# Kernel tuning notes

Measured on AMD Instinct MI355X. Metric: run time of the kernel, lower is better.

Reference implementation:

```python
import jax, jax.numpy as jnp
import numpy as np

T, B, OBS, A, P, NB, H = 32, 256, 1024, 16, 600, 601, 128


def setup_inputs() -> dict:
    key = jax.random.key(0)
    ks = jax.random.split(key, 32)
    f32 = jnp.float32

    def rn(k, shape, scale):
        return jax.random.normal(k, shape, dtype=f32) * scale

    hh = 1.0 / np.sqrt(H)
    inp = {
        "obs_seq": rn(ks[0], (T, B, OBS), 1.0),
        # backbone MLP (512, 512)
        "bb_w1": rn(ks[1], (OBS, 512), 1.0 / np.sqrt(OBS)), "bb_b1": jnp.zeros((512,), f32),
        "bb_w2": rn(ks[2], (512, 512), 1.0 / np.sqrt(512)), "bb_b2": jnp.zeros((512,), f32),
        # feedforward heads (final layers init std=0.01, bias 0 per module)
        "pol_w": rn(ks[3], (512, A), 0.01), "pol_b": jnp.zeros((A,), f32),
        "y_w": rn(ks[4], (512, P), 0.01), "y_b": jnp.zeros((P,), f32),
        "ci_w": rn(ks[5], (512, H), 1.0 / np.sqrt(512)), "ci_b": jnp.zeros((H,), f32),
        # LSTMCell(A, 128): gate order i,f,g,o as in torch
        "w_ih": rn(ks[6], (A, 4 * H), hh), "w_hh": rn(ks[7], (H, 4 * H), hh),
        "b_ih": rn(ks[8], (4 * H,), hh), "b_hh": rn(ks[9], (4 * H,), hh),
        # z / q / aux_pi MLPs: Linear(128,128) -> ReLU -> Linear(128, out)
        "z_w1": rn(ks[10], (H, H), hh), "z_b1": jnp.zeros((H,), f32),
        "z_w2": rn(ks[11], (H, P), 0.01), "z_b2": jnp.zeros((P,), f32),
        "q_w1": rn(ks[12], (H, H), hh), "q_b1": jnp.zeros((H,), f32),
        "q_w2": rn(ks[13], (H, NB), 0.01), "q_b2": jnp.zeros((NB,), f32),
        "a_w1": rn(ks[14], (H, H), hh), "a_b1": jnp.zeros((H,), f32),
        "a_w2": rn(ks[15], (H, A), 0.01), "a_b2": jnp.zeros((A,), f32),
    }
    return inp


def reference(obs_seq, bb_w1, bb_b1, bb_w2, bb_b2, pol_w, pol_b, y_w, y_b,
              ci_w, ci_b, w_ih, w_hh, b_ih, b_hh,
              z_w1, z_b1, z_w2, z_b2, q_w1, q_b1, q_w2, q_b2,
              a_w1, a_b1, a_w2, a_b2):
    Tn, Bn = obs_seq.shape[:2]
    x = obs_seq.reshape(Tn * Bn, -1)  # feedforward across time: fold T into batch
    emb = jax.nn.relu(jax.nn.relu(x @ bb_w1 + bb_b1) @ bb_w2 + bb_b2)  # [N,512]
    logits = emb @ pol_w + pol_b  # [N,A]
    y = emb @ y_w + y_b           # [N,P]
    c0 = emb @ ci_w + ci_b        # [N,H]
    h0 = jnp.tanh(c0)

    # one_hot(a) @ W_ih^T == row a of W_ih (input-to-gate contribution per action)
    in_gates = w_ih + b_ih  # [A, 4H]

    def step(carry, ig):
        h, c = carry
        g = ig + h @ w_hh + b_hh  # [N,4H]
        i, f, gg, o = jnp.split(g, 4, axis=-1)  # torch gate order i,f,g,o
        c = jax.nn.sigmoid(f) * c + jax.nn.sigmoid(i) * jnp.tanh(gg)
        h = jax.nn.sigmoid(o) * jnp.tanh(c)
        return (h, c), h

    _, h_all = jax.lax.scan(step, (h0, c0), in_gates)  # [A, N, H]

    def mlp(hx, w1, b1, w2, b2):
        return jax.nn.relu(hx @ w1 + b1) @ w2 + b2

    def to_tba(arr):
        Aa, N, D = arr.shape
        return arr.reshape(Aa, Tn, Bn, D).transpose(1, 2, 0, 3)  # [T,B,A,D]

    z = to_tba(mlp(h_all, z_w1, z_b1, z_w2, z_b2))
    q = to_tba(mlp(h_all, q_w1, q_b1, q_w2, q_b2))
    aux_pi = to_tba(mlp(h_all, a_w1, a_b1, a_w2, a_b2))
    return (logits.reshape(Tn, Bn, -1), y.reshape(Tn, Bn, -1), z, q, aux_pi)
```

## Files before the change

### kernel.cpp

```cpp
#include <hip/hip_runtime.h>
#include <stdint.h>

typedef short bf16x8 __attribute__((ext_vector_type(8)));
typedef float f32x4 __attribute__((ext_vector_type(4)));
typedef unsigned short u16x4 __attribute__((ext_vector_type(4)));

__device__ __forceinline__ unsigned short f2b(float f) {
  union { float f; unsigned u; } v; v.f = f;
  unsigned r = v.u + 0x7fffu + ((v.u >> 16) & 1u);
  return (unsigned short)(r >> 16);
}
__device__ __forceinline__ float fsigm(float x) { return 1.f / (1.f + __expf(-x)); }
__device__ __forceinline__ float ftanh(float x) {
  float t = __expf(-2.f * fabsf(x));
  float r = (1.f - t) / (1.f + t);
  return copysignf(r, x);
}

struct TD { const float* in; unsigned short* out; int R, C; };
struct TDs { TD d[12]; };

__global__ __launch_bounds__(256) void tconv_all(TDs ds) {
  TD t = ds.d[blockIdx.z];
  int c0 = blockIdx.x * 32, r0 = blockIdx.y * 32;
  if (c0 >= t.C || r0 >= t.R) return;
  __shared__ float tl[32][33];
  int tx = threadIdx.x & 31, ty = threadIdx.x >> 5;
  #pragma unroll
  for (int i = 0; i < 32; i += 8) {
    int r = r0 + ty + i, c = c0 + tx;
    tl[ty + i][tx] = (r < t.R && c < t.C) ? t.in[(size_t)r * t.C + c] : 0.f;
  }
  __syncthreads();
  #pragma unroll
  for (int i = 0; i < 32; i += 8) {
    int c = c0 + ty + i, r = r0 + tx;
    if (c < t.C && r < t.R) t.out[(size_t)c * t.R + r] = f2b(tl[tx][ty + i]);
  }
}

__global__ __launch_bounds__(256) void conv_k(const float* __restrict__ in,
                                              unsigned short* __restrict__ out, int n) {
  int i = (blockIdx.x * 256 + threadIdx.x) * 8;
  if (i >= n) return;
  float4 a = *(const float4*)(in + i);
  float4 b = *(const float4*)(in + i + 4);
  bf16x8 v;
  v[0] = (short)f2b(a.x); v[1] = (short)f2b(a.y); v[2] = (short)f2b(a.z); v[3] = (short)f2b(a.w);
  v[4] = (short)f2b(b.x); v[5] = (short)f2b(b.y); v[6] = (short)f2b(b.z); v[7] = (short)f2b(b.w);
  *(bf16x8*)(out + i) = v;
}

template <int ACT, bool OBF16>
__global__ __launch_bounds__(256) void gemm_k(const unsigned short* __restrict__ A,
                                              const unsigned short* __restrict__ BT,
                                              const float* __restrict__ bias,
                                              void* __restrict__ Cp,
                                              int M, int N, int K, int ldC) {
  __shared__ unsigned short As[64][40];
  __shared__ unsigned short Bs[64][40];
  const int tid = threadIdx.x;
  const int n0 = blockIdx.x * 64;
  const int m0 = blockIdx.y * 64;
  const int wid = tid >> 6, lane = tid & 63;
  const int wm = (wid >> 1) * 32, wn = (wid & 1) * 32;
  const int lr = lane & 15, lk = lane >> 4;
  const int sr = tid >> 2, sc = (tid & 3) * 8;

  f32x4 acc[2][2] = {};

  for (int k0 = 0; k0 < K; k0 += 32) {
    *(bf16x8*)&As[sr][sc] = *(const bf16x8*)(A + (size_t)(m0 + sr) * K + k0 + sc);
    {
      int n = n0 + sr;
      bf16x8 v = {};
      if (n < N) v = *(const bf16x8*)(BT + (size_t)n * K + k0 + sc);
      *(bf16x8*)&Bs[sr][sc] = v;
    }
    __syncthreads();
    bf16x8 af[2], bfr[2];
    #pragma unroll
    for (int mi = 0; mi < 2; mi++) af[mi] = *(const bf16x8*)&As[wm + mi * 16 + lr][lk * 8];
    #pragma unroll
    for (int ni = 0; ni < 2; ni++) bfr[ni] = *(const bf16x8*)&Bs[wn + ni * 16 + lr][lk * 8];
    #pragma unroll
    for (int mi = 0; mi < 2; mi++)
      #pragma unroll
      for (int ni = 0; ni < 2; ni++)
        acc[mi][ni] = __builtin_amdgcn_mfma_f32_16x16x32_bf16(af[mi], bfr[ni], acc[mi][ni], 0, 0, 0);
    __syncthreads();
  }

  #pragma unroll
  for (int mi = 0; mi < 2; mi++)
    #pragma unroll
    for (int ni = 0; ni < 2; ni++) {
      int col = n0 + wn + ni * 16 + lr;
      if (col >= N) continue;
      float bv = bias[col];
      #pragma unroll
      for (int r = 0; r < 4; r++) {
        int row = m0 + wm + mi * 16 + lk * 4 + r;
        float v = acc[mi][ni][r] + bv;
        if (ACT == 1) v = fmaxf(v, 0.f);
        if (OBF16) ((unsigned short*)Cp)[(size_t)row * ldC + col] = f2b(v);
        else       ((float*)Cp)[(size_t)row * ldC + col] = v;
      }
    }
}

__global__ __launch_bounds__(1024) void lstm_k(const float* __restrict__ c0,
                                               const unsigned short* __restrict__ whhT,
                                               const float* __restrict__ w_ih,
                                               const float* __restrict__ b_ih,
                                               const float* __restrict__ b_hh,
                                               unsigned short* __restrict__ h_all) {
  __shared__ float G[32][516];
  __shared__ float cst[32][128];
  __shared__ unsigned short hst[32][136];
  const int tid = threadIdx.x, lane = tid & 63, wid = tid >> 6;
  const int r0 = blockIdx.x * 32;
  const int lr = lane & 15, lk = lane >> 4;

  {
    int r = tid >> 5, j4 = (tid & 31) * 4;
    float4 c4 = *(const float4*)(c0 + (size_t)(r0 + r) * 128 + j4);
    *(f32x4*)&cst[r][j4] = f32x4{c4.x, c4.y, c4.z, c4.w};
    u16x4 h4;
    h4[0] = f2b(ftanh(c4.x)); h4[1] = f2b(ftanh(c4.y));
    h4[2] = f2b(ftanh(c4.z)); h4[3] = f2b(ftanh(c4.w));
    *(u16x4*)&hst[r][j4] = h4;
  }
  __syncthreads();

  for (int a = 0; a < 16; a++) {
    f32x4 acc[2][2] = {};
    #pragma unroll
    for (int ks = 0; ks < 4; ks++) {
      bf16x8 af0 = *(const bf16x8*)&hst[lr][ks * 32 + lk * 8];
      bf16x8 af1 = *(const bf16x8*)&hst[16 + lr][ks * 32 + lk * 8];
      #pragma unroll
      for (int nj = 0; nj < 2; nj++) {
        int col = wid * 32 + nj * 16 + lr;
        bf16x8 bv = *(const bf16x8*)(whhT + (size_t)col * 128 + ks * 32 + lk * 8);
        acc[0][nj] = __builtin_amdgcn_mfma_f32_16x16x32_bf16(af0, bv, acc[0][nj], 0, 0, 0);
        acc[1][nj] = __builtin_amdgcn_mfma_f32_16x16x32_bf16(af1, bv, acc[1][nj], 0, 0, 0);
      }
    }
    #pragma unroll
    for (int mi = 0; mi < 2; mi++)
      #pragma unroll
      for (int nj = 0; nj < 2; nj++)
        #pragma unroll
        for (int rr = 0; rr < 4; rr++)
          G[mi * 16 + lk * 4 + rr][wid * 32 + nj * 16 + lr] = acc[mi][nj][rr];
    __syncthreads();

    const float* ig = w_ih + a * 512;
    #pragma unroll
    for (int it = 0; it < 4; it++) {
      int e = tid + it * 1024;
      int r = e >> 7, j = e & 127;
      float gi = G[r][j]       + ig[j]       + b_ih[j]       + b_hh[j];
      float gf = G[r][j + 128] + ig[j + 128] + b_ih[j + 128] + b_hh[j + 128];
      float gg = G[r][j + 256] + ig[j + 256] + b_ih[j + 256] + b_hh[j + 256];
      float go = G[r][j + 384] + ig[j + 384] + b_ih[j + 384] + b_hh[j + 384];
      float c = cst[r][j];
      float cn = fsigm(gf) * c + fsigm(gi) * ftanh(gg);
      float h = fsigm(go) * ftanh(cn);
      cst[r][j] = cn;
      unsigned short hb = f2b(h);
      hst[r][j] = hb;
      h_all[((size_t)(r0 + r) * 16 + a) * 128 + j] = hb;
    }
    __syncthreads();
  }
}

__global__ __launch_bounds__(256, 4) void heads_k(
    const unsigned short* __restrict__ hall,
    const unsigned short* __restrict__ w1cat,
    const unsigned short* __restrict__ w2cat,
    const float* __restrict__ zb1, const float* __restrict__ qb1, const float* __restrict__ ab1,
    const float* __restrict__ zb2, const float* __restrict__ qb2, const float* __restrict__ ab2,
    float* __restrict__ oz, float* __restrict__ oq, float* __restrict__ oa) {
  __shared__ unsigned short hs[64][136];
  __shared__ unsigned short hd[64][136];
  const int tid = threadIdx.x;
  const int r0 = blockIdx.x * 64;
  const int lane = tid & 63, wid = tid >> 6;
  const int lr = lane & 15, lk = lane >> 4;

  {
    int row = tid >> 2, cb = (tid & 3) * 8;
    #pragma unroll
    for (int it = 0; it < 4; it++) {
      int col = cb + it * 32;
      *(bf16x8*)&hs[row][col] = *(const bf16x8*)(hall + (size_t)(r0 + row) * 128 + col);
    }
  }
  __syncthreads();

  const float* B1a[3] = {zb1, qb1, ab1};
  const float* B2a[3] = {zb2, qb2, ab2};
  float*       OOa[3] = {oz, oq, oa};

  #pragma unroll
  for (int hi = 0; hi < 3; hi++) {
    const int NF = (hi == 0) ? 38 : (hi == 1) ? 38 : 1;
    const int Nh = (hi == 0) ? 600 : (hi == 1) ? 601 : 16;
    const int so = (hi == 0) ? 0 : (hi == 1) ? 600 : 1201;
    const float* b1 = B1a[hi];
    const float* b2 = B2a[hi];
    float* Oh = OOa[hi];

    {
      bf16x8 w1v[2][4];
      #pragma unroll
      for (int j = 0; j < 2; j++) {
        int col = (wid * 2 + j) * 16 + lr;
        #pragma unroll
        for (int ks = 0; ks < 4; ks++)
          w1v[j][ks] = *(const bf16x8*)(w1cat + (size_t)(hi * 128 + col) * 128 + ks * 32 + lk * 8);
      }
      f32x4 hacc[2][4] = {};
      #pragma unroll
      for (int ks = 0; ks < 4; ks++) {
        bf16x8 av[4];
        #pragma unroll
        for (int mi = 0; mi < 4; mi++)
          av[mi] = *(const bf16x8*)&hs[mi * 16 + lr][ks * 32 + lk * 8];
        #pragma unroll
        for (int j = 0; j < 2; j++)
          #pragma unroll
          for (int mi = 0; mi < 4; mi++)
            hacc[j][mi] = __builtin_amdgcn_mfma_f32_16x16x32_bf16(av[mi], w1v[j][ks], hacc[j][mi], 0, 0, 0);
      }
      #pragma unroll
      for (int j = 0; j < 2; j++) {
        int col = (wid * 2 + j) * 16 + lr;
        float bb = b1[col];
        #pragma unroll
        for (int mi = 0; mi < 4; mi++)
          #pragma unroll
          for (int rr = 0; rr < 4; rr++)
            hd[mi * 16 + lk * 4 + rr][col] = f2b(fmaxf(hacc[j][mi][rr] + bb, 0.f));
      }
    }
    __syncthreads();

    {
      bf16x8 hda[4][4];
      #pragma unroll
      for (int mi = 0; mi < 4; mi++)
        #pragma unroll
        for (int ks = 0; ks < 4; ks++)
          hda[mi][ks] = *(const bf16x8*)&hd[mi * 16 + lr][ks * 32 + lk * 8];

      bf16x8 bvA[4], bvB[4];
      int f = wid;
      if (f < NF) {
        int bc = min(f * 16 + lr, Nh - 1);
        #pragma unroll
        for (int ks = 0; ks < 4; ks++)
          bvA[ks] = *(const bf16x8*)(w2cat + (size_t)(so + bc) * 128 + ks * 32 + lk * 8);
      }
      for (; f < NF; f += 4) {
        int fn = f + 4;
        if (fn < NF) {
          int bc = min(fn * 16 + lr, Nh - 1);
          #pragma unroll
          for (int ks = 0; ks < 4; ks++)
            bvB[ks] = *(const bf16x8*)(w2cat + (size_t)(so + bc) * 128 + ks * 32 + lk * 8);
        }
        f32x4 oacc[4] = {};
        #pragma unroll
        for (int ks = 0; ks < 4; ks++)
          #pragma unroll
          for (int mi = 0; mi < 4; mi++)
            oacc[mi] = __builtin_amdgcn_mfma_f32_16x16x32_bf16(hda[mi][ks], bvA[ks], oacc[mi], 0, 0, 0);
        int col = f * 16 + lr;
        if (col < Nh) {
          float bb = b2[col];
          #pragma unroll
          for (int mi = 0; mi < 4; mi++)
            #pragma unroll
            for (int rr = 0; rr < 4; rr++)
              Oh[(size_t)(r0 + mi * 16 + lk * 4 + rr) * Nh + col] = oacc[mi][rr] + bb;
        }
        #pragma unroll
        for (int ks = 0; ks < 4; ks++) bvA[ks] = bvB[ks];
      }
    }
    __syncthreads();
  }
}

extern "C" void kernel_launch(void* const* d_in, const int* in_sizes, int n_in,
                              void* d_out, int out_size, void* d_ws, size_t ws_size,
                              hipStream_t stream) {
  const float* obs   = (const float*)d_in[0];
  const float* bb_w1 = (const float*)d_in[1];
  const float* bb_b1 = (const float*)d_in[2];
  const float* bb_w2 = (const float*)d_in[3];
  const float* bb_b2 = (const float*)d_in[4];
  const float* pol_w = (const float*)d_in[5];
  const float* pol_b = (const float*)d_in[6];
  const float* y_w   = (const float*)d_in[7];
  const float* y_b   = (const float*)d_in[8];
  const float* ci_w  = (const float*)d_in[9];
  const float* ci_b  = (const float*)d_in[10];
  const float* w_ih  = (const float*)d_in[11];
  const float* w_hh  = (const float*)d_in[12];
  const float* b_ih  = (const float*)d_in[13];
  const float* b_hh  = (const float*)d_in[14];
  const float* z_w1  = (const float*)d_in[15];
  const float* z_b1  = (const float*)d_in[16];
  const float* z_w2  = (const float*)d_in[17];
  const float* z_b2  = (const float*)d_in[18];
  const float* q_w1  = (const float*)d_in[19];
  const float* q_b1  = (const float*)d_in[20];
  const float* q_w2  = (const float*)d_in[21];
  const float* q_b2  = (const float*)d_in[22];
  const float* a_w1  = (const float*)d_in[23];
  const float* a_b1  = (const float*)d_in[24];
  const float* a_w2  = (const float*)d_in[25];
  const float* a_b2  = (const float*)d_in[26];

  float* out = (float*)d_out;
  float* out_logits = out;
  float* out_y      = out + 131072;
  float* out_z      = out + 5046272;
  float* out_q      = out + 83689472;
  float* out_a      = out + 162463744;

  uint8_t* ws = (uint8_t*)d_ws;
  size_t off = 0;
  auto alc = [&](size_t bytes) -> void* {
    void* p = ws + off;
    off = (off + bytes + 255) & ~(size_t)255;
    return p;
  };
  unsigned short* W1T  = (unsigned short*)alc((size_t)512 * 1024 * 2);
  unsigned short* W2T  = (unsigned short*)alc((size_t)512 * 512 * 2);
  unsigned short* polT = (unsigned short*)alc((size_t)16 * 512 * 2);
  unsigned short* yT   = (unsigned short*)alc((size_t)600 * 512 * 2);
  unsigned short* ciT  = (unsigned short*)alc((size_t)128 * 512 * 2);
  unsigned short* whhT = (unsigned short*)alc((size_t)512 * 128 * 2);
  unsigned short* zw1T = (unsigned short*)alc((size_t)128 * 128 * 2);
  unsigned short* qw1T = (unsigned short*)alc((size_t)128 * 128 * 2);
  unsigned short* aw1T = (unsigned short*)alc((size_t)128 * 128 * 2);
  unsigned short* zw2T = (unsigned short*)alc((size_t)600 * 128 * 2);
  unsigned short* qw2T = (unsigned short*)alc((size_t)601 * 128 * 2);
  unsigned short* aw2T = (unsigned short*)alc((size_t)16 * 128 * 2);
  unsigned short* obsb = (unsigned short*)alc((size_t)8192 * 1024 * 2);
  unsigned short* hid1 = (unsigned short*)alc((size_t)8192 * 512 * 2);
  unsigned short* emb  = (unsigned short*)alc((size_t)8192 * 512 * 2);
  float*          c0b  = (float*)alc((size_t)8192 * 128 * 4);
  unsigned short* hall = (unsigned short*)alc((size_t)8192 * 16 * 128 * 2);
  (void)ws_size; (void)in_sizes; (void)n_in; (void)out_size;

  dim3 B256(256);

  TDs td;
  td.d[0]  = {bb_w1, W1T, 1024, 512};
  td.d[1]  = {bb_w2, W2T, 512, 512};
  td.d[2]  = {pol_w, polT, 512, 16};
  td.d[3]  = {y_w,   yT,   512, 600};
  td.d[4]  = {ci_w,  ciT,  512, 128};
  td.d[5]  = {w_hh,  whhT, 128, 512};
  td.d[6]  = {z_w1,  zw1T, 128, 128};
  td.d[7]  = {z_w2,  zw2T, 128, 600};
  td.d[8]  = {q_w1,  qw1T, 128, 128};
  td.d[9]  = {q_w2,  qw2T, 128, 601};
  td.d[10] = {a_w1,  aw1T, 128, 128};
  td.d[11] = {a_w2,  aw2T, 128, 16};
  tconv_all<<<dim3(19, 32, 12), B256, 0, stream>>>(td);

  conv_k<<<dim3(4096), B256, 0, stream>>>(obs, obsb, 8192 * 1024);

  gemm_k<1, true><<<dim3(8, 128), B256, 0, stream>>>(obsb, W1T, bb_b1, hid1, 8192, 512, 1024, 512);
  gemm_k<1, true><<<dim3(8, 128), B256, 0, stream>>>(hid1, W2T, bb_b2, emb,  8192, 512, 512,  512);
  gemm_k<0, false><<<dim3(1, 128),  B256, 0, stream>>>(emb, polT, pol_b, out_logits, 8192, 16,  512, 16);
  gemm_k<0, false><<<dim3(10, 128), B256, 0, stream>>>(emb, yT,   y_b,   out_y,      8192, 600, 512, 600);
  gemm_k<0, false><<<dim3(2, 128),  B256, 0, stream>>>(emb, ciT,  ci_b,  c0b,        8192, 128, 512, 128);
  lstm_k<<<dim3(256), dim3(1024), 0, stream>>>(c0b, whhT, w_ih, b_ih, b_hh, hall);
  heads_k<<<dim3(2048), B256, 0, stream>>>(hall,
                                           zw1T, zw2T,
                                           z_b1, q_b1, a_b1,
                                           z_b2, q_b2, a_b2,
                                           out_z, out_q, out_a);
}
```

Before: 481.7 us.

## Restructure heads kernel to single-wave blocks with transposed MFMA and vector stores

The LSTM kernel now keeps its W_hh fragments in registers across all 16 steps and precomputes the bias sums and per-step input-gate values per thread. The heads kernel is rebuilt around 64-thread blocks, each handling 32 rows. Each block reads h directly from global memory, swaps the MFMA operand order so every lane produces 4 contiguous output columns, and writes those with 16-byte vector stores instead of scattered scalar stores. It also drops the block-level barriers in favour of a wave-local LDS wait. The cost is more blocks, with each block reloading W1 and W2, and more VGPR pressure from the register-resident weights.

```diff
diff --git a/kernel.cpp b/kernel.cpp
--- a/kernel.cpp
+++ b/kernel.cpp
@@ -122,6 +122,20 @@
   const int r0 = blockIdx.x * 32;
   const int lr = lane & 15, lk = lane >> 4;
 
+  bf16x8 wv[2][4];
+  #pragma unroll
+  for (int nj = 0; nj < 2; nj++)
+    #pragma unroll
+    for (int ks = 0; ks < 4; ks++)
+      wv[nj][ks] = *(const bf16x8*)(whhT + (size_t)(wid * 32 + nj * 16 + lr) * 128 + ks * 32 + lk * 8);
+
+  const int j = tid & 127;
+  const int rb = tid >> 7;
+  const float bs0 = b_ih[j]       + b_hh[j];
+  const float bs1 = b_ih[j + 128] + b_hh[j + 128];
+  const float bs2 = b_ih[j + 256] + b_hh[j + 256];
+  const float bs3 = b_ih[j + 384] + b_hh[j + 384];
+
   {
     int r = tid >> 5, j4 = (tid & 31) * 4;
     float4 c4 = *(const float4*)(c0 + (size_t)(r0 + r) * 128 + j4);
@@ -141,10 +155,8 @@
       bf16x8 af1 = *(const bf16x8*)&hst[16 + lr][ks * 32 + lk * 8];
       #pragma unroll
       for (int nj = 0; nj < 2; nj++) {
-        int col = wid * 32 + nj * 16 + lr;
-        bf16x8 bv = *(const bf16x8*)(whhT + (size_t)col * 128 + ks * 32 + lk * 8);
-        acc[0][nj] = __builtin_amdgcn_mfma_f32_16x16x32_bf16(af0, bv, acc[0][nj], 0, 0, 0);
-        acc[1][nj] = __builtin_amdgcn_mfma_f32_16x16x32_bf16(af1, bv, acc[1][nj], 0, 0, 0);
+        acc[0][nj] = __builtin_amdgcn_mfma_f32_16x16x32_bf16(af0, wv[nj][ks], acc[0][nj], 0, 0, 0);
+        acc[1][nj] = __builtin_amdgcn_mfma_f32_16x16x32_bf16(af1, wv[nj][ks], acc[1][nj], 0, 0, 0);
       }
     }
     #pragma unroll
@@ -157,14 +169,14 @@
     __syncthreads();
 
     const float* ig = w_ih + a * 512;
+    const float ig0 = ig[j], ig1 = ig[j + 128], ig2 = ig[j + 256], ig3 = ig[j + 384];
     #pragma unroll
     for (int it = 0; it < 4; it++) {
-      int e = tid + it * 1024;
-      int r = e >> 7, j = e & 127;
-      float gi = G[r][j]       + ig[j]       + b_ih[j]       + b_hh[j];
-      float gf = G[r][j + 128] + ig[j + 128] + b_ih[j + 128] + b_hh[j + 128];
-      float gg = G[r][j + 256] + ig[j + 256] + b_ih[j + 256] + b_hh[j + 256];
-      float go = G[r][j + 384] + ig[j + 384] + b_ih[j + 384] + b_hh[j + 384];
+      int r = rb + it * 8;
+      float gi = G[r][j]       + ig0 + bs0;
+      float gf = G[r][j + 128] + ig1 + bs1;
+      float gg = G[r][j + 256] + ig2 + bs2;
+      float go = G[r][j + 384] + ig3 + bs3;
       float c = cst[r][j];
       float cn = fsigm(gf) * c + fsigm(gi) * ftanh(gg);
       float h = fsigm(go) * ftanh(cn);
@@ -177,29 +189,17 @@
   }
 }
 
-__global__ __launch_bounds__(256, 4) void heads_k(
+__global__ __launch_bounds__(64, 4) void heads_k(
     const unsigned short* __restrict__ hall,
     const unsigned short* __restrict__ w1cat,
     const unsigned short* __restrict__ w2cat,
     const float* __restrict__ zb1, const float* __restrict__ qb1, const float* __restrict__ ab1,
     const float* __restrict__ zb2, const float* __restrict__ qb2, const float* __restrict__ ab2,
     float* __restrict__ oz, float* __restrict__ oq, float* __restrict__ oa) {
-  __shared__ unsigned short hs[64][136];
-  __shared__ unsigned short hd[64][136];
-  const int tid = threadIdx.x;
-  const int r0 = blockIdx.x * 64;
-  const int lane = tid & 63, wid = tid >> 6;
+  __shared__ unsigned short hp[32][136];
+  const int lane = threadIdx.x & 63;
   const int lr = lane & 15, lk = lane >> 4;
-
-  {
-    int row = tid >> 2, cb = (tid & 3) * 8;
-    #pragma unroll
-    for (int it = 0; it < 4; it++) {
-      int col = cb + it * 32;
-      *(bf16x8*)&hs[row][col] = *(const bf16x8*)(hall + (size_t)(r0 + row) * 128 + col);
-    }
-  }
-  __syncthreads();
+  const int r0 = blockIdx.x * 32;
 
   const float* B1a[3] = {zb1, qb1, ab1};
   const float* B2a[3] = {zb2, qb2, ab2};
@@ -207,92 +207,102 @@
 
   #pragma unroll
   for (int hi = 0; hi < 3; hi++) {
-    const int NF = (hi == 0) ? 38 : (hi == 1) ? 38 : 1;
-    const int Nh = (hi == 0) ? 600 : (hi == 1) ? 601 : 16;
-    const int so = (hi == 0) ? 0 : (hi == 1) ? 600 : 1201;
+    const int Nh    = (hi == 0) ? 600 : (hi == 1) ? 601 : 16;
+    const int so    = (hi == 0) ? 0 : (hi == 1) ? 600 : 1201;
+    const int NFULL = Nh >> 4;
+    const int TAIL  = Nh & 15;
     const float* b1 = B1a[hi];
     const float* b2 = B2a[hi];
     float* Oh = OOa[hi];
 
     {
-      bf16x8 w1v[2][4];
-      #pragma unroll
-      for (int j = 0; j < 2; j++) {
-        int col = (wid * 2 + j) * 16 + lr;
+      bf16x8 av[2][4];
+      #pragma unroll
+      for (int jf = 0; jf < 2; jf++)
         #pragma unroll
         for (int ks = 0; ks < 4; ks++)
-          w1v[j][ks] = *(const bf16x8*)(w1cat + (size_t)(hi * 128 + col) * 128 + ks * 32 + lk * 8);
-      }
-      f32x4 hacc[2][4] = {};
-      #pragma unroll
-      for (int ks = 0; ks < 4; ks++) {
-        bf16x8 av[4];
-        #pragma unroll
-        for (int mi = 0; mi < 4; mi++)
-          av[mi] = *(const bf16x8*)&hs[mi * 16 + lr][ks * 32 + lk * 8];
-        #pragma unroll
-        for (int j = 0; j < 2; j++)
+          av[jf][ks] = *(const bf16x8*)(hall + (size_t)(r0 + jf * 16 + lr) * 128 + ks * 32 + lk * 8);
+      #pragma unroll
+      for (int nf = 0; nf < 8; nf++) {
+        bf16x8 w1v[4];
+        #pragma unroll
+        for (int ks = 0; ks < 4; ks++)
+          w1v[ks] = *(const bf16x8*)(w1cat + (size_t)(hi * 128 + nf * 16 + lr) * 128 + ks * 32 + lk * 8);
+        f32x4 hacc[2] = {};
+        #pragma unroll
+        for (int ks = 0; ks < 4; ks++)
           #pragma unroll
-          for (int mi = 0; mi < 4; mi++)
-            hacc[j][mi] = __builtin_amdgcn_mfma_f32_16x16x32_bf16(av[mi], w1v[j][ks], hacc[j][mi], 0, 0, 0);
-      }
-      #pragma unroll
-      for (int j = 0; j < 2; j++) {
-        int col = (wid * 2 + j) * 16 + lr;
-        float bb = b1[col];
-        #pragma unroll
-        for (int mi = 0; mi < 4; mi++)
+          for (int jf = 0; jf < 2; jf++)
+            hacc[jf] = __builtin_amdgcn_mfma_f32_16x16x32_bf16(w1v[ks], av[jf][ks], hacc[jf], 0, 0, 0);
+        f32x4 bb = *(const f32x4*)(b1 + nf * 16 + lk * 4);
+        #pragma unroll
+        for (int jf = 0; jf < 2; jf++) {
+          u16x4 h4;
           #pragma unroll
           for (int rr = 0; rr < 4; rr++)
-            hd[mi * 16 + lk * 4 + rr][col] = f2b(fmaxf(hacc[j][mi][rr] + bb, 0.f));
+            h4[rr] = f2b(fmaxf(hacc[jf][rr] + bb[rr], 0.f));
+          *(u16x4*)&hp[jf * 16 + lr][nf * 16 + lk * 4] = h4;
+        }
       }
     }
-    __syncthreads();
-
+    asm volatile("s_waitcnt lgkmcnt(0)" ::: "memory");
+    __builtin_amdgcn_sched_barrier(0);
+
+    bf16x8 hv[2][4];
+    #pragma unroll
+    for (int jf = 0; jf < 2; jf++)
+      #pragma unroll
+      for (int ks = 0; ks < 4; ks++)
+        hv[jf][ks] = *(const bf16x8*)&hp[jf * 16 + lr][ks * 32 + lk * 8];
+
+    bf16x8 wA[4], wB[4];
     {
-      bf16x8 hda[4][4];
-      #pragma unroll
-      for (int mi = 0; mi < 4; mi++)
+      int rowb = min(lr, Nh - 1);
+      #pragma unroll
+      for (int ks = 0; ks < 4; ks++)
+        wA[ks] = *(const bf16x8*)(w2cat + (size_t)(so + rowb) * 128 + ks * 32 + lk * 8);
+    }
+    const int NFT = NFULL + (TAIL ? 1 : 0);
+    for (int fo = 0; fo < NFULL; fo++) {
+      int fn = fo + 1;
+      if (fn < NFT) {
+        int rowb = min(fn * 16 + lr, Nh - 1);
         #pragma unroll
         for (int ks = 0; ks < 4; ks++)
-          hda[mi][ks] = *(const bf16x8*)&hd[mi * 16 + lr][ks * 32 + lk * 8];
-
-      bf16x8 bvA[4], bvB[4];
-      int f = wid;
-      if (f < NF) {
-        int bc = min(f * 16 + lr, Nh - 1);
-        #pragma unroll
-        for (int ks = 0; ks < 4; ks++)
-          bvA[ks] = *(const bf16x8*)(w2cat + (size_t)(so + bc) * 128 + ks * 32 + lk * 8);
+          wB[ks] = *(const bf16x8*)(w2cat + (size_t)(so + rowb) * 128 + ks * 32 + lk * 8);
       }
-      for (; f < NF; f += 4) {
-        int fn = f + 4;
-        if (fn < NF) {
-          int bc = min(fn * 16 + lr, Nh - 1);
-          #pragma unroll
-          for (int ks = 0; ks < 4; ks++)
-            bvB[ks] = *(const bf16x8*)(w2cat + (size_t)(so + bc) * 128 + ks * 32 + lk * 8);
+      f32x4 oacc[2] = {};
+      #pragma unroll
+      for (int ks = 0; ks < 4; ks++)
+        #pragma unroll
+        for (int jf = 0; jf < 2; jf++)
+          oacc[jf] = __builtin_amdgcn_mfma_f32_16x16x32_bf16(wA[ks], hv[jf][ks], oacc[jf], 0, 0, 0);
+      f32x4 bb = *(const f32x4*)(b2 + fo * 16 + lk * 4);
+      #pragma unroll
+      for (int jf = 0; jf < 2; jf++) {
+        f32x4 v = oacc[jf] + bb;
+        float* p = Oh + (size_t)(r0 + jf * 16 + lr) * Nh + fo * 16 + lk * 4;
+        __builtin_memcpy(p, &v, 16);
+      }
+      #pragma unroll
+      for (int ks = 0; ks < 4; ks++) wA[ks] = wB[ks];
+    }
+    if (TAIL) {
+      f32x4 oacc[2] = {};
+      #pragma unroll
+      for (int ks = 0; ks < 4; ks++)
+        #pragma unroll
+        for (int jf = 0; jf < 2; jf++)
+          oacc[jf] = __builtin_amdgcn_mfma_f32_16x16x32_bf16(wA[ks], hv[jf][ks], oacc[jf], 0, 0, 0);
+      #pragma unroll
+      for (int jf = 0; jf < 2; jf++)
+        #pragma unroll
+        for (int rr = 0; rr < 4; rr++) {
+          int col = NFULL * 16 + lk * 4 + rr;
+          if (col < Nh)
+            Oh[(size_t)(r0 + jf * 16 + lr) * Nh + col] = oacc[jf][rr] + b2[col];
         }
-        f32x4 oacc[4] = {};
-        #pragma unroll
-        for (int ks = 0; ks < 4; ks++)
-          #pragma unroll
-          for (int mi = 0; mi < 4; mi++)
-            oacc[mi] = __builtin_amdgcn_mfma_f32_16x16x32_bf16(hda[mi][ks], bvA[ks], oacc[mi], 0, 0, 0);
-        int col = f * 16 + lr;
-        if (col < Nh) {
-          float bb = b2[col];
-          #pragma unroll
-          for (int mi = 0; mi < 4; mi++)
-            #pragma unroll
-            for (int rr = 0; rr < 4; rr++)
-              Oh[(size_t)(r0 + mi * 16 + lk * 4 + rr) * Nh + col] = oacc[mi][rr] + bb;
-        }
-        #pragma unroll
-        for (int ks = 0; ks < 4; ks++) bvA[ks] = bvB[ks];
-      }
-    }
-    __syncthreads();
+    }
   }
 }
 
@@ -385,9 +395,9 @@
   gemm_k<0, false><<<dim3(10, 128), B256, 0, stream>>>(emb, yT,   y_b,   out_y,      8192, 600, 512, 600);
   gemm_k<0, false><<<dim3(2, 128),  B256, 0, stream>>>(emb, ciT,  ci_b,  c0b,        8192, 128, 512, 128);
   lstm_k<<<dim3(256), dim3(1024), 0, stream>>>(c0b, whhT, w_ih, b_ih, b_hh, hall);
-  heads_k<<<dim3(2048), B256, 0, stream>>>(hall,
-                                           zw1T, zw2T,
-                                           z_b1, q_b1, a_b1,
-                                           z_b2, q_b2, a_b2,
-                                           out_z, out_q, out_a);
-}
+  heads_k<<<dim3(4096), dim3(64), 0, stream>>>(hall,
+                                               zw1T, zw2T,
+                                               z_b1, q_b1, a_b1,
+                                               z_b2, q_b2, a_b2,
+                                               out_z, out_q, out_a);
+}
```

Result: slower. 506.7 us (+5.2%).
